# Kernel tuning notes

Hardware: AMD Instinct MI355X
Metric: run time of the kernel (lower is better)

The kernel has to match this reference:

```python
import jax, jax.numpy as jnp
import numpy as np

NB, B, IN, HID = 8, 256, 512, 512
G = 4 * HID
WB, IB, ABNM = 8, 8, 8
NL = 0.05


def quant(x, bits, r):
    # QuantFunc.forward: scale, clamp to (-1+1/step, 1-1/step), round to step grid, rescale
    step = 2.0 ** (bits - 1)
    x01 = jnp.clip(x / r, -1.0 + 1.0 / step, 1.0 - 1.0 / step)
    return jnp.round(x01 * step) / step * r


def pact(x, a):
    # pact_a_bmm vectorized over the block dim: sign(x)*0.5*(|x| - ||x|-a| + a)
    a3 = a[:, None, None]
    return jnp.sign(x) * 0.5 * (jnp.abs(x) - jnp.abs(jnp.abs(x) - a3) + a3)


def custom_mm(inp, w, b, nw, nb):
    # CustomMM_bmm.forward: quantize weights/bias (range 1.0), add scaled noise, bmm
    wq = quant(w, WB, 1.0)
    bq = quant(b, WB, 1.0)
    out = jnp.einsum('bni,bio->bno', inp, wq + nw * jnp.max(w) * NL)
    return out + bq + nb * jnp.max(b) * NL


def setup_inputs():
    key = jax.random.key(0)
    ks = jax.random.split(key, 11)
    inp = {
        'input': jax.random.normal(ks[0], (B, IN), jnp.float32),
        'hx': jax.random.normal(ks[1], (NB, B, HID), jnp.float32),
        'cx': jax.random.normal(ks[2], (NB, B, HID), jnp.float32),
        'weight_ih': jax.random.normal(ks[3], (NB, IN, G), jnp.float32),
        'weight_hh': jax.random.normal(ks[4], (NB, HID, G), jnp.float32),
        'bias_ih': jax.random.normal(ks[5], (NB, 1, G), jnp.float32),
        'bias_hh': jax.random.normal(ks[6], (NB, 1, G), jnp.float32),
        'noise_wih': jax.random.normal(ks[7], (NB, IN, G), jnp.float32),
        'noise_whh': jax.random.normal(ks[8], (NB, HID, G), jnp.float32),
        'noise_bih': jax.random.normal(ks[9], (NB, 1, G), jnp.float32),
        'noise_bhh': jax.random.normal(ks[10], (NB, 1, G), jnp.float32),
        'a1': jnp.full((NB,), 128.0, jnp.float32),
        'a3': jnp.ones((NB,), jnp.float32),
        'a4': jnp.ones((NB,), jnp.float32),
        'a5': jnp.ones((NB,), jnp.float32),
        'a6': jnp.ones((NB,), jnp.float32),
        'a7': jnp.full((NB,), 4.0, jnp.float32),
        'a8': jnp.ones((NB,), jnp.float32),
        'a9': jnp.full((NB,), 4.0, jnp.float32),
        'a10': jnp.ones((NB,), jnp.float32),
        'a11': jnp.full((NB,), 4.0, jnp.float32),
    }
    return inp


def reference(input, hx, cx, weight_ih, weight_hh, bias_ih, bias_hh,
              noise_wih, noise_whh, noise_bih, noise_bhh,
              a1, a3, a4, a5, a6, a7, a8, a9, a10, a11):
    xr = jnp.broadcast_to(input[None], (NB,) + input.shape)  # input.repeat(n_blocks,1,1)
    xq = quant(pact(xr, a1), IB, a1[:, None, None])
    gates = custom_mm(xq, weight_ih, bias_ih, noise_wih, noise_bih) \
          + custom_mm(hx, weight_hh, bias_hh, noise_whh, noise_bhh)
    i, j, f, o = jnp.split(gates, 4, axis=2)
    qp = lambda x, a: quant(pact(x, a), ABNM, a[:, None, None])
    fg = qp(jax.nn.sigmoid(f), a3)
    ig = qp(jax.nn.sigmoid(i), a4)
    act = qp(jnp.tanh(j), a5)
    og = qp(jax.nn.sigmoid(o), a6)
    gated = qp(cx * fg, a7)
    actin = qp(ig * act, a8)
    new_c = qp(gated + actin, a9)
    actc = qp(jnp.tanh(new_c), a10)
    new_h = qp(actc * og, a11)
    return new_h, new_c
```

## Files before the change

### kernel.cpp

```cpp
#include <hip/hip_runtime.h>
#include <hip/hip_bf16.h>

#define NBATCH 8
#define BROWS 256
#define KDIM 512
#define HIDD 512
#define GDIM 2048

typedef float f32x4 __attribute__((ext_vector_type(4)));
typedef __bf16 bf16x8 __attribute__((ext_vector_type(8)));

__device__ __forceinline__ unsigned fenc(float f) {
    unsigned u = __float_as_uint(f);
    return (u & 0x80000000u) ? ~u : (u | 0x80000000u);
}
__device__ __forceinline__ float fdec(unsigned e) {
    unsigned u = (e & 0x80000000u) ? (e & 0x7fffffffu) : ~e;
    return __uint_as_float(u);
}
__device__ __forceinline__ unsigned umaxu(unsigned a, unsigned b) { return a > b ? a : b; }

__device__ __forceinline__ float qpact(float x, float a) {
    float ax = fabsf(x);
    float p  = copysignf(0.5f * (ax - fabsf(ax - a) + a), x);
    float x01 = p / a;
    x01 = fminf(fmaxf(x01, -0.9921875f), 0.9921875f);
    return (rintf(x01 * 128.f) * 0.0078125f) * a;
}
__device__ __forceinline__ float q1(float x) {
    float x01 = fminf(fmaxf(x, -0.9921875f), 0.9921875f);
    return rintf(x01 * 128.f) * 0.0078125f;
}
__device__ __forceinline__ float sigmf(float x) { return 1.0f / (1.0f + expf(-x)); }

__global__ void k_init(unsigned* m) { if (threadIdx.x < 4) m[threadIdx.x] = 0u; }

__global__ void k_max(const float* __restrict__ w_ih, const float* __restrict__ w_hh,
                      const float* __restrict__ b_ih, const float* __restrict__ b_hh,
                      unsigned* __restrict__ omax) {
    int which = blockIdx.y;
    const float* src = which == 0 ? w_ih : which == 1 ? w_hh : which == 2 ? b_ih : b_hh;
    int n4 = (which < 2 ? NBATCH * KDIM * GDIM : NBATCH * GDIM) >> 2;
    unsigned best = 0u;
    int stride = gridDim.x * blockDim.x;
    for (int i = blockIdx.x * blockDim.x + threadIdx.x; i < n4; i += stride) {
        float4 v = ((const float4*)src)[i];
        best = umaxu(best, fenc(v.x)); best = umaxu(best, fenc(v.y));
        best = umaxu(best, fenc(v.z)); best = umaxu(best, fenc(v.w));
    }
    #pragma unroll
    for (int off = 32; off > 0; off >>= 1)
        best = umaxu(best, (unsigned)__shfl_down((int)best, off, 64));
    __shared__ unsigned red[4];
    int lane = threadIdx.x & 63, wv = threadIdx.x >> 6;
    if (lane == 0) red[wv] = best;
    __syncthreads();
    if (threadIdx.x == 0) {
        unsigned b2 = umaxu(umaxu(red[0], red[1]), umaxu(red[2], red[3]));
        atomicMax(&omax[which], b2);
    }
}

__global__ void k_prep(const float* __restrict__ input, const float* __restrict__ hx,
                       const float* __restrict__ bih, const float* __restrict__ bhh,
                       const float* __restrict__ nbih, const float* __restrict__ nbhh,
                       const float* __restrict__ a1, const unsigned* __restrict__ maxes,
                       __hip_bfloat16* __restrict__ xqh, __hip_bfloat16* __restrict__ hxh,
                       __hip_bfloat16* __restrict__ hxl, float* __restrict__ bias_comb) {
    const int NX = NBATCH * BROWS * KDIM;
    const int NH = NBATCH * BROWS * HIDD;
    const int NBC = NBATCH * GDIM;
    int total = NX + NH + NBC;
    int stride = gridDim.x * blockDim.x;
    for (int i = blockIdx.x * blockDim.x + threadIdx.x; i < total; i += stride) {
        if (i < NX) {
            int nb = i >> 17;
            int rem = i & 131071;
            float v = qpact(input[rem], a1[nb]);
            xqh[i] = __float2bfloat16(v);
        } else if (i < NX + NH) {
            int j = i - NX;
            float h = hx[j];
            __hip_bfloat16 hi = __float2bfloat16(h);
            hxh[j] = hi;
            hxl[j] = __float2bfloat16(h - __bfloat162float(hi));
        } else {
            int j = i - NX - NH;
            float mb_ih = fdec(maxes[2]);
            float mb_hh = fdec(maxes[3]);
            bias_comb[j] = q1(bih[j]) + (nbih[j] * mb_ih) * 0.05f
                         + q1(bhh[j]) + (nbhh[j] * mb_hh) * 0.05f;
        }
    }
}

__global__ __launch_bounds__(512) void k_gemm(
    const float* __restrict__ w_ih, const float* __restrict__ w_hh,
    const float* __restrict__ n_ih, const float* __restrict__ n_hh,
    const __hip_bfloat16* __restrict__ xqh, const __hip_bfloat16* __restrict__ hxh,
    const __hip_bfloat16* __restrict__ hxl,
    const float* __restrict__ bias_comb, const float* __restrict__ cx,
    const float* __restrict__ a3, const float* __restrict__ a4, const float* __restrict__ a5,
    const float* __restrict__ a6, const float* __restrict__ a7, const float* __restrict__ a8,
    const float* __restrict__ a9, const float* __restrict__ a10, const float* __restrict__ a11,
    const unsigned* __restrict__ maxes,
    float* __restrict__ out_h, float* __restrict__ out_c)
{
    __shared__ __hip_bfloat16 Bsm[4][64][40];

    int tid = threadIdx.x;
    int lane = tid & 63, wv = tid >> 6;
    int nb = blockIdx.x >> 5;
    int cb = blockIdx.x & 31;

    const float* wih_b = w_ih + nb * KDIM * GDIM;
    const float* whh_b = w_hh + nb * KDIM * GDIM;
    const float* nih_b = n_ih + nb * KDIM * GDIM;
    const float* nhh_b = n_hh + nb * KDIM * GDIM;
    const __hip_bfloat16* xq_b = xqh + nb * BROWS * KDIM;
    const __hip_bfloat16* hh_b = hxh + nb * BROWS * KDIM;
    const __hip_bfloat16* hl_b = hxl + nb * BROWS * KDIM;

    float c_ih = fdec(maxes[0]);
    float c_hh = fdec(maxes[1]);

    f32x4 acc[2][4] = {};

    int lh = lane & 15;
    int lk = (lane >> 4) << 3;
    int m0 = wv << 5;

    for (int k0 = 0; k0 < KDIM; k0 += 32) {
        __syncthreads();
        #pragma unroll
        for (int t = 0; t < 4; ++t) {
            int id = tid + (t << 9);
            int n = id & 63;
            int k = id >> 6;
            int g = n >> 4;
            int col = (g << 9) + (cb << 4) + (n & 15);
            int gidx = (k0 + k) * GDIM + col;
            float w1 = wih_b[gidx], z1 = nih_b[gidx];
            float wq1 = rintf(fminf(fmaxf(w1, -0.9921875f), 0.9921875f) * 128.f) * 0.0078125f;
            float e1 = wq1 + (z1 * c_ih) * 0.05f;
            __hip_bfloat16 h1 = __float2bfloat16(e1);
            Bsm[0][n][k] = h1;
            Bsm[1][n][k] = __float2bfloat16(e1 - __bfloat162float(h1));
            float w2 = whh_b[gidx], z2 = nhh_b[gidx];
            float wq2 = rintf(fminf(fmaxf(w2, -0.9921875f), 0.9921875f) * 128.f) * 0.0078125f;
            float e2 = wq2 + (z2 * c_hh) * 0.05f;
            __hip_bfloat16 h2 = __float2bfloat16(e2);
            Bsm[2][n][k] = h2;
            Bsm[3][n][k] = __float2bfloat16(e2 - __bfloat162float(h2));
        }
        __syncthreads();

        bf16x8 ax[2], ah[2], al[2];
        #pragma unroll
        for (int mf = 0; mf < 2; ++mf) {
            int r = m0 + (mf << 4) + lh;
            int aoff = r * KDIM + k0 + lk;
            ax[mf] = *(const bf16x8*)(xq_b + aoff);
            ah[mf] = *(const bf16x8*)(hh_b + aoff);
            al[mf] = *(const bf16x8*)(hl_b + aoff);
        }
        bf16x8 b0[4], b1[4], b2[4], b3[4];
        #pragma unroll
        for (int nf = 0; nf < 4; ++nf) {
            int n = (nf << 4) + lh;
            b0[nf] = *(const bf16x8*)&Bsm[0][n][lk];
            b1[nf] = *(const bf16x8*)&Bsm[1][n][lk];
            b2[nf] = *(const bf16x8*)&Bsm[2][n][lk];
            b3[nf] = *(const bf16x8*)&Bsm[3][n][lk];
        }
        #pragma unroll
        for (int mf = 0; mf < 2; ++mf)
            #pragma unroll
            for (int nf = 0; nf < 4; ++nf) {
                acc[mf][nf] = __builtin_amdgcn_mfma_f32_16x16x32_bf16(ax[mf], b0[nf], acc[mf][nf], 0, 0, 0);
                acc[mf][nf] = __builtin_amdgcn_mfma_f32_16x16x32_bf16(ax[mf], b1[nf], acc[mf][nf], 0, 0, 0);
                acc[mf][nf] = __builtin_amdgcn_mfma_f32_16x16x32_bf16(ah[mf], b2[nf], acc[mf][nf], 0, 0, 0);
                acc[mf][nf] = __builtin_amdgcn_mfma_f32_16x16x32_bf16(ah[mf], b3[nf], acc[mf][nf], 0, 0, 0);
                acc[mf][nf] = __builtin_amdgcn_mfma_f32_16x16x32_bf16(al[mf], b2[nf], acc[mf][nf], 0, 0, 0);
            }
    }

    int hcol = (cb << 4) + lh;
    float A3 = a3[nb], A4 = a4[nb], A5 = a5[nb], A6 = a6[nb], A7 = a7[nb];
    float A8 = a8[nb], A9 = a9[nb], A10 = a10[nb], A11 = a11[nb];
    float bc_i = bias_comb[nb * GDIM + hcol];
    float bc_j = bias_comb[nb * GDIM + 512 + hcol];
    float bc_f = bias_comb[nb * GDIM + 1024 + hcol];
    float bc_o = bias_comb[nb * GDIM + 1536 + hcol];
    #pragma unroll
    for (int mf = 0; mf < 2; ++mf)
        #pragma unroll
        for (int rg = 0; rg < 4; ++rg) {
            int r = m0 + (mf << 4) + ((lane >> 4) << 2) + rg;
            float gi = acc[mf][0][rg] + bc_i;
            float gj = acc[mf][1][rg] + bc_j;
            float gf = acc[mf][2][rg] + bc_f;
            float go = acc[mf][3][rg] + bc_o;
            float fg = qpact(sigmf(gf), A3);
            float ig = qpact(sigmf(gi), A4);
            float act = qpact(tanhf(gj), A5);
            float og = qpact(sigmf(go), A6);
            int oidx = (nb * BROWS + r) * HIDD + hcol;
            float cv = cx[oidx];
            float gated = qpact(cv * fg, A7);
            float actin = qpact(ig * act, A8);
            float ncv = qpact(gated + actin, A9);
            float acv = qpact(tanhf(ncv), A10);
            float nhv = qpact(acv * og, A11);
            out_h[oidx] = nhv;
            out_c[oidx] = ncv;
        }
}

extern "C" void kernel_launch(void* const* d_in, const int* in_sizes, int n_in,
                              void* d_out, int out_size, void* d_ws, size_t ws_size,
                              hipStream_t stream) {
    const float* input = (const float*)d_in[0];
    const float* hx    = (const float*)d_in[1];
    const float* cx    = (const float*)d_in[2];
    const float* w_ih  = (const float*)d_in[3];
    const float* w_hh  = (const float*)d_in[4];
    const float* b_ih  = (const float*)d_in[5];
    const float* b_hh  = (const float*)d_in[6];
    const float* n_wih = (const float*)d_in[7];
    const float* n_whh = (const float*)d_in[8];
    const float* n_bih = (const float*)d_in[9];
    const float* n_bhh = (const float*)d_in[10];
    const float* a1  = (const float*)d_in[11];
    const float* a3  = (const float*)d_in[12];
    const float* a4  = (const float*)d_in[13];
    const float* a5  = (const float*)d_in[14];
    const float* a6  = (const float*)d_in[15];
    const float* a7  = (const float*)d_in[16];
    const float* a8  = (const float*)d_in[17];
    const float* a9  = (const float*)d_in[18];
    const float* a10 = (const float*)d_in[19];
    const float* a11 = (const float*)d_in[20];

    float* out_h = (float*)d_out;
    float* out_c = out_h + NBATCH * BROWS * HIDD;

    char* ws = (char*)d_ws;
    unsigned* maxes = (unsigned*)ws;
    __hip_bfloat16* xqh = (__hip_bfloat16*)(ws + 256);
    __hip_bfloat16* hxh = (__hip_bfloat16*)(ws + 256 + 2097152);
    __hip_bfloat16* hxl = (__hip_bfloat16*)(ws + 256 + 2 * 2097152);
    float* bias_comb    = (float*)(ws + 256 + 3 * 2097152);

    k_init<<<1, 64, 0, stream>>>(maxes);
    k_max<<<dim3(256, 4), 256, 0, stream>>>(w_ih, w_hh, b_ih, b_hh, maxes);
    k_prep<<<2048, 256, 0, stream>>>(input, hx, b_ih, b_hh, n_bih, n_bhh, a1, maxes,
                                     xqh, hxh, hxl, bias_comb);
    k_gemm<<<NBATCH * 32, 512, 0, stream>>>(w_ih, w_hh, n_wih, n_whh, xqh, hxh, hxl,
                                            bias_comb, cx,
                                            a3, a4, a5, a6, a7, a8, a9, a10, a11,
                                            maxes, out_h, out_c);
}
```

Before: 97.91 us.

## Double-buffer weight staging with register prefetch and vectorized float4 loads in k_gemm

Reworks the GEMM main loop so weight and noise tiles are loaded as float4 vectors into registers two k-steps ahead. They are then quantized into one of two shared-memory buffers, so only one barrier is needed per k-step instead of two. The block index mapping is also swapped so that consecutive blocks cover different NB batches, and launch bounds now request two blocks per CU. The aim is to hide global-load latency behind the MFMA work, at the cost of doubled LDS use and higher register pressure.

```diff
diff --git a/kernel.cpp b/kernel.cpp
--- a/kernel.cpp
+++ b/kernel.cpp
@@ -6,6 +6,8 @@
 #define KDIM 512
 #define HIDD 512
 #define GDIM 2048
+#define KSTEP 32
+#define NIT (KDIM / KSTEP)
 
 typedef float f32x4 __attribute__((ext_vector_type(4)));
 typedef __bf16 bf16x8 __attribute__((ext_vector_type(8)));
@@ -94,7 +96,7 @@
     }
 }
 
-__global__ __launch_bounds__(512) void k_gemm(
+__global__ __launch_bounds__(512, 2) void k_gemm(
     const float* __restrict__ w_ih, const float* __restrict__ w_hh,
     const float* __restrict__ n_ih, const float* __restrict__ n_hh,
     const __hip_bfloat16* __restrict__ xqh, const __hip_bfloat16* __restrict__ hxh,
@@ -106,12 +108,12 @@
     const unsigned* __restrict__ maxes,
     float* __restrict__ out_h, float* __restrict__ out_c)
 {
-    __shared__ __hip_bfloat16 Bsm[4][64][40];
+    __shared__ __hip_bfloat16 Bsm[2][4][64][40];
 
     int tid = threadIdx.x;
     int lane = tid & 63, wv = tid >> 6;
-    int nb = blockIdx.x >> 5;
-    int cb = blockIdx.x & 31;
+    int nb = blockIdx.x & 7;
+    int cb = blockIdx.x >> 3;
 
     const float* wih_b = w_ih + nb * KDIM * GDIM;
     const float* whh_b = w_hh + nb * KDIM * GDIM;
@@ -130,59 +132,79 @@
     int lk = (lane >> 4) << 3;
     int m0 = wv << 5;
 
-    for (int k0 = 0; k0 < KDIM; k0 += 32) {
+    int sn0 = (tid & 15) << 2;
+    int sk  = tid >> 4;
+    int scol = ((sn0 >> 4) << 9) + (cb << 4) + (sn0 & 15);
+    int sbase = sk * GDIM + scol;
+
+    f32x4 rw1a, rz1a, rw2a, rz2a;
+    f32x4 rw1b, rz1b, rw2b, rz2b;
+    bf16x8 axv[2], ahv[2], alv[2];
+
+#define STAGE(RW1, RZ1, RW2, RZ2, K0) {            \
+    int gx = sbase + (K0) * GDIM;                  \
+    RW1 = *(const f32x4*)(wih_b + gx);             \
+    RZ1 = *(const f32x4*)(nih_b + gx);             \
+    RW2 = *(const f32x4*)(whh_b + gx);             \
+    RZ2 = *(const f32x4*)(nhh_b + gx); }
+
+#define ALOAD(K0) {                                \
+    _Pragma("unroll")                              \
+    for (int mf = 0; mf < 2; ++mf) {               \
+        int aoff = (m0 + (mf << 4) + lh) * KDIM + (K0) + lk; \
+        axv[mf] = *(const bf16x8*)(xq_b + aoff);   \
+        ahv[mf] = *(const bf16x8*)(hh_b + aoff);   \
+        alv[mf] = *(const bf16x8*)(hl_b + aoff); } }
+
+#define CVT(P, RW1, RZ1, RW2, RZ2) {               \
+    _Pragma("unroll")                              \
+    for (int j = 0; j < 4; ++j) {                  \
+        float w1 = RW1[j], z1 = RZ1[j];            \
+        float wq1 = rintf(fminf(fmaxf(w1, -0.9921875f), 0.9921875f) * 128.f) * 0.0078125f; \
+        float e1 = wq1 + (z1 * c_ih) * 0.05f;      \
+        __hip_bfloat16 h1 = __float2bfloat16(e1);  \
+        Bsm[P][0][sn0 + j][sk] = h1;               \
+        Bsm[P][1][sn0 + j][sk] = __float2bfloat16(e1 - __bfloat162float(h1)); \
+        float w2 = RW2[j], z2 = RZ2[j];            \
+        float wq2 = rintf(fminf(fmaxf(w2, -0.9921875f), 0.9921875f) * 128.f) * 0.0078125f; \
+        float e2 = wq2 + (z2 * c_hh) * 0.05f;      \
+        __hip_bfloat16 h2 = __float2bfloat16(e2);  \
+        Bsm[P][2][sn0 + j][sk] = h2;               \
+        Bsm[P][3][sn0 + j][sk] = __float2bfloat16(e2 - __bfloat162float(h2)); \
+    } }
+
+#define COMPUTE(P) {                               \
+    _Pragma("unroll")                              \
+    for (int nf = 0; nf < 4; ++nf) {               \
+        int n = (nf << 4) + lh;                    \
+        bf16x8 b0 = *(const bf16x8*)&Bsm[P][0][n][lk]; \
+        bf16x8 b1 = *(const bf16x8*)&Bsm[P][1][n][lk]; \
+        bf16x8 b2 = *(const bf16x8*)&Bsm[P][2][n][lk]; \
+        bf16x8 b3 = *(const bf16x8*)&Bsm[P][3][n][lk]; \
+        _Pragma("unroll")                          \
+        for (int mf = 0; mf < 2; ++mf) {           \
+            acc[mf][nf] = __builtin_amdgcn_mfma_f32_16x16x32_bf16(axv[mf], b0, acc[mf][nf], 0, 0, 0); \
+            acc[mf][nf] = __builtin_amdgcn_mfma_f32_16x16x32_bf16(axv[mf], b1, acc[mf][nf], 0, 0, 0); \
+            acc[mf][nf] = __builtin_amdgcn_mfma_f32_16x16x32_bf16(ahv[mf], b2, acc[mf][nf], 0, 0, 0); \
+            acc[mf][nf] = __builtin_amdgcn_mfma_f32_16x16x32_bf16(ahv[mf], b3, acc[mf][nf], 0, 0, 0); \
+            acc[mf][nf] = __builtin_amdgcn_mfma_f32_16x16x32_bf16(alv[mf], b2, acc[mf][nf], 0, 0, 0); \
+        } \
+    } }
+
+    STAGE(rw1a, rz1a, rw2a, rz2a, 0);
+    STAGE(rw1b, rz1b, rw2b, rz2b, KSTEP);
+
+    for (int it = 0; it < NIT; it += 2) {
+        ALOAD(it * KSTEP);
+        CVT(0, rw1a, rz1a, rw2a, rz2a);
+        if (it + 2 < NIT) STAGE(rw1a, rz1a, rw2a, rz2a, (it + 2) * KSTEP);
         __syncthreads();
-        #pragma unroll
-        for (int t = 0; t < 4; ++t) {
-            int id = tid + (t << 9);
-            int n = id & 63;
-            int k = id >> 6;
-            int g = n >> 4;
-            int col = (g << 9) + (cb << 4) + (n & 15);
-            int gidx = (k0 + k) * GDIM + col;
-            float w1 = wih_b[gidx], z1 = nih_b[gidx];
-            float wq1 = rintf(fminf(fmaxf(w1, -0.9921875f), 0.9921875f) * 128.f) * 0.0078125f;
-            float e1 = wq1 + (z1 * c_ih) * 0.05f;
-            __hip_bfloat16 h1 = __float2bfloat16(e1);
-            Bsm[0][n][k] = h1;
-            Bsm[1][n][k] = __float2bfloat16(e1 - __bfloat162float(h1));
-            float w2 = whh_b[gidx], z2 = nhh_b[gidx];
-            float wq2 = rintf(fminf(fmaxf(w2, -0.9921875f), 0.9921875f) * 128.f) * 0.0078125f;
-            float e2 = wq2 + (z2 * c_hh) * 0.05f;
-            __hip_bfloat16 h2 = __float2bfloat16(e2);
-            Bsm[2][n][k] = h2;
-            Bsm[3][n][k] = __float2bfloat16(e2 - __bfloat162float(h2));
-        }
+        COMPUTE(0);
+        ALOAD((it + 1) * KSTEP);
+        CVT(1, rw1b, rz1b, rw2b, rz2b);
+        if (it + 3 < NIT) STAGE(rw1b, rz1b, rw2b, rz2b, (it + 3) * KSTEP);
         __syncthreads();
-
-        bf16x8 ax[2], ah[2], al[2];
-        #pragma unroll
-        for (int mf = 0; mf < 2; ++mf) {
-            int r = m0 + (mf << 4) + lh;
-            int aoff = r * KDIM + k0 + lk;
-            ax[mf] = *(const bf16x8*)(xq_b + aoff);
-            ah[mf] = *(const bf16x8*)(hh_b + aoff);
-            al[mf] = *(const bf16x8*)(hl_b + aoff);
-        }
-        bf16x8 b0[4], b1[4], b2[4], b3[4];
-        #pragma unroll
-        for (int nf = 0; nf < 4; ++nf) {
-            int n = (nf << 4) + lh;
-            b0[nf] = *(const bf16x8*)&Bsm[0][n][lk];
-            b1[nf] = *(const bf16x8*)&Bsm[1][n][lk];
-            b2[nf] = *(const bf16x8*)&Bsm[2][n][lk];
-            b3[nf] = *(const bf16x8*)&Bsm[3][n][lk];
-        }
-        #pragma unroll
-        for (int mf = 0; mf < 2; ++mf)
-            #pragma unroll
-            for (int nf = 0; nf < 4; ++nf) {
-                acc[mf][nf] = __builtin_amdgcn_mfma_f32_16x16x32_bf16(ax[mf], b0[nf], acc[mf][nf], 0, 0, 0);
-                acc[mf][nf] = __builtin_amdgcn_mfma_f32_16x16x32_bf16(ax[mf], b1[nf], acc[mf][nf], 0, 0, 0);
-                acc[mf][nf] = __builtin_amdgcn_mfma_f32_16x16x32_bf16(ah[mf], b2[nf], acc[mf][nf], 0, 0, 0);
-                acc[mf][nf] = __builtin_amdgcn_mfma_f32_16x16x32_bf16(ah[mf], b3[nf], acc[mf][nf], 0, 0, 0);
-                acc[mf][nf] = __builtin_amdgcn_mfma_f32_16x16x32_bf16(al[mf], b2[nf], acc[mf][nf], 0, 0, 0);
-            }
+        COMPUTE(1);
     }
 
     int hcol = (cb << 4) + lh;
```

New measurement: 80.19 us. 18.1% less time.

## Warp-specialize GEMM with producer waves double-buffering weight conversion into LDS

Applied to the files above, without the earlier changes.

Splits each 1024-thread block into 8 producer waves, which load, quantize and split weights into a double-buffered LDS tile, and 8 consumer waves, which run 32x32x16 MFMAs on the previous tile. Global weight loads and conversion now overlap with matrix math, and KSTEP goes to 64. The block-to-tile mapping is swizzled so adjacent blocks cover different batches, and the init kernel becomes a memset. The epilogue uses cross-lane shuffles to regroup gate columns. The risk is that a single 1024-thread block per CU limits occupancy and adds register pressure.

```diff
diff --git a/kernel.cpp b/kernel.cpp
--- a/kernel.cpp
+++ b/kernel.cpp
@@ -6,8 +6,11 @@
 #define KDIM 512
 #define HIDD 512
 #define GDIM 2048
+#define KSTEP 64
+#define NIT (KDIM / KSTEP)
 
 typedef float f32x4 __attribute__((ext_vector_type(4)));
+typedef float f32x16 __attribute__((ext_vector_type(16)));
 typedef __bf16 bf16x8 __attribute__((ext_vector_type(8)));
 
 __device__ __forceinline__ unsigned fenc(float f) {
@@ -32,8 +35,6 @@
     return rintf(x01 * 128.f) * 0.0078125f;
 }
 __device__ __forceinline__ float sigmf(float x) { return 1.0f / (1.0f + expf(-x)); }
-
-__global__ void k_init(unsigned* m) { if (threadIdx.x < 4) m[threadIdx.x] = 0u; }
 
 __global__ void k_max(const float* __restrict__ w_ih, const float* __restrict__ w_hh,
                       const float* __restrict__ b_ih, const float* __restrict__ b_hh,
@@ -94,7 +95,7 @@
     }
 }
 
-__global__ __launch_bounds__(512) void k_gemm(
+__global__ __launch_bounds__(1024, 1) void k_gemm(
     const float* __restrict__ w_ih, const float* __restrict__ w_hh,
     const float* __restrict__ n_ih, const float* __restrict__ n_hh,
     const __hip_bfloat16* __restrict__ xqh, const __hip_bfloat16* __restrict__ hxh,
@@ -106,12 +107,12 @@
     const unsigned* __restrict__ maxes,
     float* __restrict__ out_h, float* __restrict__ out_c)
 {
-    __shared__ __hip_bfloat16 Bsm[4][64][40];
+    __shared__ __hip_bfloat16 Bsm[2][4][64][72];
 
     int tid = threadIdx.x;
     int lane = tid & 63, wv = tid >> 6;
-    int nb = blockIdx.x >> 5;
-    int cb = blockIdx.x & 31;
+    int nb = blockIdx.x & 7;
+    int cb = blockIdx.x >> 3;
 
     const float* wih_b = w_ih + nb * KDIM * GDIM;
     const float* whh_b = w_hh + nb * KDIM * GDIM;
@@ -124,88 +125,128 @@
     float c_ih = fdec(maxes[0]);
     float c_hh = fdec(maxes[1]);
 
-    f32x4 acc[2][4] = {};
-
-    int lh = lane & 15;
-    int lk = (lane >> 4) << 3;
-    int m0 = wv << 5;
-
-    for (int k0 = 0; k0 < KDIM; k0 += 32) {
-        __syncthreads();
-        #pragma unroll
-        for (int t = 0; t < 4; ++t) {
-            int id = tid + (t << 9);
-            int n = id & 63;
-            int k = id >> 6;
-            int g = n >> 4;
-            int col = (g << 9) + (cb << 4) + (n & 15);
-            int gidx = (k0 + k) * GDIM + col;
-            float w1 = wih_b[gidx], z1 = nih_b[gidx];
-            float wq1 = rintf(fminf(fmaxf(w1, -0.9921875f), 0.9921875f) * 128.f) * 0.0078125f;
-            float e1 = wq1 + (z1 * c_ih) * 0.05f;
-            __hip_bfloat16 h1 = __float2bfloat16(e1);
-            Bsm[0][n][k] = h1;
-            Bsm[1][n][k] = __float2bfloat16(e1 - __bfloat162float(h1));
-            float w2 = whh_b[gidx], z2 = nhh_b[gidx];
-            float wq2 = rintf(fminf(fmaxf(w2, -0.9921875f), 0.9921875f) * 128.f) * 0.0078125f;
-            float e2 = wq2 + (z2 * c_hh) * 0.05f;
-            __hip_bfloat16 h2 = __float2bfloat16(e2);
-            Bsm[2][n][k] = h2;
-            Bsm[3][n][k] = __float2bfloat16(e2 - __bfloat162float(h2));
+    bool producer = wv >= 8;
+
+    int pn = lane;
+    int po = (wv - 8) & 7;
+    int ps = pn >> 4;
+    int gm = (int)((0x3120u >> (ps << 2)) & 0xFu);
+    int pcol = (gm << 9) + (cb << 4) + (pn & 15);
+
+    int cw = wv & 7;
+    int c31 = lane & 31;
+    int ck8 = (lane >> 5) << 3;
+
+    f32x16 acc0 = {}, acc1 = {};
+    float rw1[8], rz1[8], rw2[8], rz2[8];
+
+#define PSTAGE(K0) {                                         \
+    int kb = (K0) + (po << 3);                               \
+    _Pragma("unroll")                                        \
+    for (int j = 0; j < 8; ++j) {                            \
+        int gx = (kb + j) * GDIM + pcol;                     \
+        rw1[j] = wih_b[gx]; rz1[j] = nih_b[gx];              \
+        rw2[j] = whh_b[gx]; rz2[j] = nhh_b[gx];              \
+    } }
+
+#define PCVT1(P, RW, RZ, CM, MHI) {                          \
+    bf16x8 hi8, lo8;                                         \
+    _Pragma("unroll")                                        \
+    for (int j = 0; j < 8; ++j) {                            \
+        float w = RW[j];                                     \
+        float wq = rintf(fminf(fmaxf(w, -0.9921875f), 0.9921875f) * 128.f) * 0.0078125f; \
+        float e = wq + (RZ[j] * (CM)) * 0.05f;               \
+        __hip_bfloat16 h = __float2bfloat16(e);              \
+        float lof = e - __bfloat162float(h);                 \
+        __hip_bfloat16 lb = __float2bfloat16(lof);           \
+        hi8[j] = *reinterpret_cast<__bf16*>(&h);             \
+        lo8[j] = *reinterpret_cast<__bf16*>(&lb);            \
+    }                                                        \
+    *(bf16x8*)&Bsm[P][MHI][pn][po << 3] = hi8;               \
+    *(bf16x8*)&Bsm[P][(MHI) + 1][pn][po << 3] = lo8; }
+
+#define MFMA5(ACC, AX, AH, AL, B0, B1, B2, B3)                                \
+    ACC = __builtin_amdgcn_mfma_f32_32x32x16_bf16(AX, B0, ACC, 0, 0, 0);      \
+    ACC = __builtin_amdgcn_mfma_f32_32x32x16_bf16(AX, B1, ACC, 0, 0, 0);      \
+    ACC = __builtin_amdgcn_mfma_f32_32x32x16_bf16(AH, B2, ACC, 0, 0, 0);      \
+    ACC = __builtin_amdgcn_mfma_f32_32x32x16_bf16(AH, B3, ACC, 0, 0, 0);      \
+    ACC = __builtin_amdgcn_mfma_f32_32x32x16_bf16(AL, B2, ACC, 0, 0, 0);
+
+    if (producer) PSTAGE(0);
+
+    for (int ph = 0; ph <= NIT; ++ph) {
+        if (producer) {
+            if (ph < NIT) {
+                int P = ph & 1;
+                PCVT1(P, rw1, rz1, c_ih, 0);
+                PCVT1(P, rw2, rz2, c_hh, 2);
+                if (ph + 1 < NIT) PSTAGE((ph + 1) * KSTEP);
+            }
+        } else if (ph > 0) {
+            int K0 = (ph - 1) * KSTEP;
+            int P = (ph - 1) & 1;
+            bf16x8 ax[4], ah[4], al[4];
+            int abase = (cw * 32 + c31) * KDIM + K0 + ck8;
+            #pragma unroll
+            for (int kc = 0; kc < 4; ++kc) {
+                ax[kc] = *(const bf16x8*)(xq_b + abase + kc * 16);
+                ah[kc] = *(const bf16x8*)(hh_b + abase + kc * 16);
+                al[kc] = *(const bf16x8*)(hl_b + abase + kc * 16);
+            }
+            #pragma unroll
+            for (int kc = 0; kc < 4; ++kc) {
+                int kb = kc * 16 + ck8;
+                {
+                    bf16x8 b0 = *(const bf16x8*)&Bsm[P][0][c31][kb];
+                    bf16x8 b1 = *(const bf16x8*)&Bsm[P][1][c31][kb];
+                    bf16x8 b2 = *(const bf16x8*)&Bsm[P][2][c31][kb];
+                    bf16x8 b3 = *(const bf16x8*)&Bsm[P][3][c31][kb];
+                    MFMA5(acc0, ax[kc], ah[kc], al[kc], b0, b1, b2, b3);
+                }
+                {
+                    bf16x8 b0 = *(const bf16x8*)&Bsm[P][0][32 + c31][kb];
+                    bf16x8 b1 = *(const bf16x8*)&Bsm[P][1][32 + c31][kb];
+                    bf16x8 b2 = *(const bf16x8*)&Bsm[P][2][32 + c31][kb];
+                    bf16x8 b3 = *(const bf16x8*)&Bsm[P][3][32 + c31][kb];
+                    MFMA5(acc1, ax[kc], ah[kc], al[kc], b0, b1, b2, b3);
+                }
+            }
         }
         __syncthreads();
-
-        bf16x8 ax[2], ah[2], al[2];
+    }
+
+    if (!producer) {
+        float recv0[16], recv1[16];
         #pragma unroll
-        for (int mf = 0; mf < 2; ++mf) {
-            int r = m0 + (mf << 4) + lh;
-            int aoff = r * KDIM + k0 + lk;
-            ax[mf] = *(const bf16x8*)(xq_b + aoff);
-            ah[mf] = *(const bf16x8*)(hh_b + aoff);
-            al[mf] = *(const bf16x8*)(hl_b + aoff);
+        for (int r = 0; r < 16; ++r) {
+            recv0[r] = __shfl_xor(acc0[r], 16);
+            recv1[r] = __shfl_xor(acc1[r], 16);
         }
-        bf16x8 b0[4], b1[4], b2[4], b3[4];
+        int hcol = (cb << 4) + (lane & 15);
+        int hi = (lane >> 4) & 1;
+        float A3 = a3[nb], A4 = a4[nb], A5 = a5[nb], A6 = a6[nb], A7 = a7[nb];
+        float A8 = a8[nb], A9 = a9[nb], A10 = a10[nb], A11 = a11[nb];
+        float bc_i = bias_comb[nb * GDIM + hcol];
+        float bc_j = bias_comb[nb * GDIM + 512 + hcol];
+        float bc_f = bias_comb[nb * GDIM + 1024 + hcol];
+        float bc_o = bias_comb[nb * GDIM + 1536 + hcol];
+        int rbase = 16 * hi + 4 * (lane >> 5);
         #pragma unroll
-        for (int nf = 0; nf < 4; ++nf) {
-            int n = (nf << 4) + lh;
-            b0[nf] = *(const bf16x8*)&Bsm[0][n][lk];
-            b1[nf] = *(const bf16x8*)&Bsm[1][n][lk];
-            b2[nf] = *(const bf16x8*)&Bsm[2][n][lk];
-            b3[nf] = *(const bf16x8*)&Bsm[3][n][lk];
-        }
-        #pragma unroll
-        for (int mf = 0; mf < 2; ++mf)
-            #pragma unroll
-            for (int nf = 0; nf < 4; ++nf) {
-                acc[mf][nf] = __builtin_amdgcn_mfma_f32_16x16x32_bf16(ax[mf], b0[nf], acc[mf][nf], 0, 0, 0);
-                acc[mf][nf] = __builtin_amdgcn_mfma_f32_16x16x32_bf16(ax[mf], b1[nf], acc[mf][nf], 0, 0, 0);
-                acc[mf][nf] = __builtin_amdgcn_mfma_f32_16x16x32_bf16(ah[mf], b2[nf], acc[mf][nf], 0, 0, 0);
-                acc[mf][nf] = __builtin_amdgcn_mfma_f32_16x16x32_bf16(ah[mf], b3[nf], acc[mf][nf], 0, 0, 0);
-                acc[mf][nf] = __builtin_amdgcn_mfma_f32_16x16x32_bf16(al[mf], b2[nf], acc[mf][nf], 0, 0, 0);
-            }
-    }
-
-    int hcol = (cb << 4) + lh;
-    float A3 = a3[nb], A4 = a4[nb], A5 = a5[nb], A6 = a6[nb], A7 = a7[nb];
-    float A8 = a8[nb], A9 = a9[nb], A10 = a10[nb], A11 = a11[nb];
-    float bc_i = bias_comb[nb * GDIM + hcol];
-    float bc_j = bias_comb[nb * GDIM + 512 + hcol];
-    float bc_f = bias_comb[nb * GDIM + 1024 + hcol];
-    float bc_o = bias_comb[nb * GDIM + 1536 + hcol];
-    #pragma unroll
-    for (int mf = 0; mf < 2; ++mf)
-        #pragma unroll
-        for (int rg = 0; rg < 4; ++rg) {
-            int r = m0 + (mf << 4) + ((lane >> 4) << 2) + rg;
-            float gi = acc[mf][0][rg] + bc_i;
-            float gj = acc[mf][1][rg] + bc_j;
-            float gf = acc[mf][2][rg] + bc_f;
-            float go = acc[mf][3][rg] + bc_o;
+        for (int r = 0; r < 8; ++r) {
+            float a0s = hi ? acc0[r + 8] : acc0[r];
+            float a1s = hi ? acc1[r + 8] : acc1[r];
+            float r0s = hi ? recv0[r + 8] : recv0[r];
+            float r1s = hi ? recv1[r + 8] : recv1[r];
+            float gi = (hi ? r0s : a0s) + bc_i;
+            float gj = (hi ? r1s : a1s) + bc_j;
+            float gf = (hi ? a0s : r0s) + bc_f;
+            float go = (hi ? a1s : r1s) + bc_o;
+            int row = cw * 32 + rbase + (r & 3) + 8 * (r >> 2);
             float fg = qpact(sigmf(gf), A3);
             float ig = qpact(sigmf(gi), A4);
             float act = qpact(tanhf(gj), A5);
             float og = qpact(sigmf(go), A6);
-            int oidx = (nb * BROWS + r) * HIDD + hcol;
+            int oidx = (nb * BROWS + row) * HIDD + hcol;
             float cv = cx[oidx];
             float gated = qpact(cv * fg, A7);
             float actin = qpact(ig * act, A8);
@@ -215,6 +256,7 @@
             out_h[oidx] = nhv;
             out_c[oidx] = ncv;
         }
+    }
 }
 
 extern "C" void kernel_launch(void* const* d_in, const int* in_sizes, int n_in,
@@ -252,12 +294,12 @@
     __hip_bfloat16* hxl = (__hip_bfloat16*)(ws + 256 + 2 * 2097152);
     float* bias_comb    = (float*)(ws + 256 + 3 * 2097152);
 
-    k_init<<<1, 64, 0, stream>>>(maxes);
+    hipMemsetAsync(maxes, 0, 16, stream);
     k_max<<<dim3(256, 4), 256, 0, stream>>>(w_ih, w_hh, b_ih, b_hh, maxes);
     k_prep<<<2048, 256, 0, stream>>>(input, hx, b_ih, b_hh, n_bih, n_bhh, a1, maxes,
                                      xqh, hxh, hxl, bias_comb);
-    k_gemm<<<NBATCH * 32, 512, 0, stream>>>(w_ih, w_hh, n_wih, n_whh, xqh, hxh, hxl,
-                                            bias_comb, cx,
-                                            a3, a4, a5, a6, a7, a8, a9, a10, a11,
-                                            maxes, out_h, out_c);
-}
+    k_gemm<<<NBATCH * 32, 1024, 0, stream>>>(w_ih, w_hh, n_wih, n_whh, xqh, hxh, hxl,
+                                             bias_comb, cx,
+                                             a3, a4, a5, a6, a7, a8, a9, a10, a11,
+                                             maxes, out_h, out_c);
+}
```

Result: faster. 93.07 us (-4.9%).

## Prepack quantized weights into tiled bf16 buffer and double-buffer GEMM via LDS loads

Applied to the files above, without the earlier changes.

Moves the weight quantize, noise add and hi/lo bf16 split out of the GEMM into a separate pack kernel that writes a tiled, padded layout to workspace. The GEMM then streams those tiles with global_load_lds into double-buffered shared memory, uses 32x32x16 MFMAs, and stages results through LDS for a coalesced epilogue. The max-reduction and activation prep kernels are merged and the init kernel becomes a memset. This adds an extra write and read of a packed weight buffer (about 32 MB of bf16) in exchange for a GEMM main loop with no fp32 weight reads or conversion.

```diff
diff --git a/kernel.cpp b/kernel.cpp
--- a/kernel.cpp
+++ b/kernel.cpp
@@ -7,8 +7,26 @@
 #define HIDD 512
 #define GDIM 2048
 
+#define ROWB 144
+#define MATSZ (64 * ROWB)
+#define PCHUNK (4 * MATSZ)
+#define NPH 8
+
+#define WS_XQH 256
+#define WS_HXH (256 + 2097152)
+#define WS_HXL (256 + 2 * 2097152)
+#define WS_BIAS (256 + 3 * 2097152)
+#define WS_P (256 + 3 * 2097152 + 65536)
+
 typedef float f32x4 __attribute__((ext_vector_type(4)));
+typedef float f32x16 __attribute__((ext_vector_type(16)));
 typedef __bf16 bf16x8 __attribute__((ext_vector_type(8)));
+typedef unsigned int u32;
+
+__device__ __forceinline__ void gload16(const void* g, void* l) {
+    __builtin_amdgcn_global_load_lds((const __attribute__((address_space(1))) u32*)g,
+                                     (__attribute__((address_space(3))) u32*)l, 16, 0, 0);
+}
 
 __device__ __forceinline__ unsigned fenc(float f) {
     unsigned u = __float_as_uint(f);
@@ -33,159 +51,216 @@
 }
 __device__ __forceinline__ float sigmf(float x) { return 1.0f / (1.0f + expf(-x)); }
 
-__global__ void k_init(unsigned* m) { if (threadIdx.x < 4) m[threadIdx.x] = 0u; }
-
-__global__ void k_max(const float* __restrict__ w_ih, const float* __restrict__ w_hh,
-                      const float* __restrict__ b_ih, const float* __restrict__ b_hh,
-                      unsigned* __restrict__ omax) {
-    int which = blockIdx.y;
-    const float* src = which == 0 ? w_ih : which == 1 ? w_hh : which == 2 ? b_ih : b_hh;
-    int n4 = (which < 2 ? NBATCH * KDIM * GDIM : NBATCH * GDIM) >> 2;
-    unsigned best = 0u;
+__global__ void k_maxprep(const float* __restrict__ w_ih, const float* __restrict__ w_hh,
+                          const float* __restrict__ b_ih, const float* __restrict__ b_hh,
+                          const float* __restrict__ input, const float* __restrict__ hx,
+                          const float* __restrict__ a1,
+                          unsigned* __restrict__ maxes,
+                          __hip_bfloat16* __restrict__ xqh, __hip_bfloat16* __restrict__ hxh,
+                          __hip_bfloat16* __restrict__ hxl) {
+    int y = blockIdx.y;
     int stride = gridDim.x * blockDim.x;
-    for (int i = blockIdx.x * blockDim.x + threadIdx.x; i < n4; i += stride) {
-        float4 v = ((const float4*)src)[i];
-        best = umaxu(best, fenc(v.x)); best = umaxu(best, fenc(v.y));
-        best = umaxu(best, fenc(v.z)); best = umaxu(best, fenc(v.w));
-    }
-    #pragma unroll
-    for (int off = 32; off > 0; off >>= 1)
-        best = umaxu(best, (unsigned)__shfl_down((int)best, off, 64));
-    __shared__ unsigned red[4];
-    int lane = threadIdx.x & 63, wv = threadIdx.x >> 6;
-    if (lane == 0) red[wv] = best;
-    __syncthreads();
-    if (threadIdx.x == 0) {
-        unsigned b2 = umaxu(umaxu(red[0], red[1]), umaxu(red[2], red[3]));
-        atomicMax(&omax[which], b2);
-    }
-}
-
-__global__ void k_prep(const float* __restrict__ input, const float* __restrict__ hx,
-                       const float* __restrict__ bih, const float* __restrict__ bhh,
-                       const float* __restrict__ nbih, const float* __restrict__ nbhh,
-                       const float* __restrict__ a1, const unsigned* __restrict__ maxes,
-                       __hip_bfloat16* __restrict__ xqh, __hip_bfloat16* __restrict__ hxh,
-                       __hip_bfloat16* __restrict__ hxl, float* __restrict__ bias_comb) {
-    const int NX = NBATCH * BROWS * KDIM;
-    const int NH = NBATCH * BROWS * HIDD;
-    const int NBC = NBATCH * GDIM;
-    int total = NX + NH + NBC;
-    int stride = gridDim.x * blockDim.x;
-    for (int i = blockIdx.x * blockDim.x + threadIdx.x; i < total; i += stride) {
-        if (i < NX) {
-            int nb = i >> 17;
-            int rem = i & 131071;
-            float v = qpact(input[rem], a1[nb]);
-            xqh[i] = __float2bfloat16(v);
-        } else if (i < NX + NH) {
-            int j = i - NX;
-            float h = hx[j];
-            __hip_bfloat16 hi = __float2bfloat16(h);
-            hxh[j] = hi;
-            hxl[j] = __float2bfloat16(h - __bfloat162float(hi));
-        } else {
-            int j = i - NX - NH;
-            float mb_ih = fdec(maxes[2]);
-            float mb_hh = fdec(maxes[3]);
-            bias_comb[j] = q1(bih[j]) + (nbih[j] * mb_ih) * 0.05f
-                         + q1(bhh[j]) + (nbhh[j] * mb_hh) * 0.05f;
-        }
-    }
-}
-
-__global__ __launch_bounds__(512) void k_gemm(
+    int gtid = blockIdx.x * blockDim.x + threadIdx.x;
+    if (y < 4) {
+        const float* src = y == 0 ? w_ih : y == 1 ? w_hh : y == 2 ? b_ih : b_hh;
+        int n4 = (y < 2 ? NBATCH * KDIM * GDIM : NBATCH * GDIM) >> 2;
+        unsigned best = 0u;
+        for (int i = gtid; i < n4; i += stride) {
+            float4 v = ((const float4*)src)[i];
+            best = umaxu(best, fenc(v.x)); best = umaxu(best, fenc(v.y));
+            best = umaxu(best, fenc(v.z)); best = umaxu(best, fenc(v.w));
+        }
+        #pragma unroll
+        for (int off = 32; off > 0; off >>= 1)
+            best = umaxu(best, (unsigned)__shfl_down((int)best, off, 64));
+        __shared__ unsigned red[4];
+        int lane = threadIdx.x & 63, wv = threadIdx.x >> 6;
+        if (lane == 0) red[wv] = best;
+        __syncthreads();
+        if (threadIdx.x == 0) {
+            unsigned b2 = umaxu(umaxu(red[0], red[1]), umaxu(red[2], red[3]));
+            atomicMax(&maxes[y], b2);
+        }
+    } else {
+        const int NX = NBATCH * BROWS * KDIM;
+        const int NH = NBATCH * BROWS * HIDD;
+        int total = NX + NH;
+        for (int i = gtid; i < total; i += stride) {
+            if (i < NX) {
+                int nb = i >> 17;
+                int rem = i & 131071;
+                float v = qpact(input[rem], a1[nb]);
+                xqh[i] = __float2bfloat16(v);
+            } else {
+                int j = i - NX;
+                float h = hx[j];
+                __hip_bfloat16 hi = __float2bfloat16(h);
+                hxh[j] = hi;
+                hxl[j] = __float2bfloat16(h - __bfloat162float(hi));
+            }
+        }
+    }
+}
+
+__global__ __launch_bounds__(1024) void k_pack(
     const float* __restrict__ w_ih, const float* __restrict__ w_hh,
     const float* __restrict__ n_ih, const float* __restrict__ n_hh,
+    const float* __restrict__ b_ih, const float* __restrict__ b_hh,
+    const float* __restrict__ nbih, const float* __restrict__ nbhh,
+    const unsigned* __restrict__ maxes,
+    char* __restrict__ P, float* __restrict__ bias_comb) {
+    int bid = blockIdx.x;
+    if (bid == 256) {
+        float mb_ih = fdec(maxes[2]);
+        float mb_hh = fdec(maxes[3]);
+        #pragma unroll
+        for (int it = 0; it < 16; ++it) {
+            int j = it * 1024 + threadIdx.x;
+            bias_comb[j] = q1(b_ih[j]) + (nbih[j] * mb_ih) * 0.05f
+                         + q1(b_hh[j]) + (nbhh[j] * mb_hh) * 0.05f;
+        }
+        return;
+    }
+    int nb = bid >> 5;
+    int p  = (bid >> 1) & 15;
+    int ch = bid & 1;
+    int k0 = p * 32;
+    int ph = p >> 1;
+    int half = p & 1;
+    float c_ih = fdec(maxes[0]);
+    float c_hh = fdec(maxes[1]);
+
+    int c = ch * 1024 + threadIdx.x;
+    int g  = c >> 9;
+    int cw = c & 511;
+    int cb = cw >> 4;
+    int cc = cw & 15;
+    int n  = (g << 4) + cc;
+
+    char* rowP = P + ((size_t)((nb * 32 + cb) * 8 + ph)) * PCHUNK + n * ROWB + half * 64;
+    size_t boff = (size_t)nb * KDIM * GDIM;
+
+    #pragma unroll
+    for (int pair = 0; pair < 2; ++pair) {
+        const float* W = (pair ? w_hh : w_ih) + boff;
+        const float* Z = (pair ? n_hh : n_ih) + boff;
+        float cm = pair ? c_hh : c_ih;
+        char* dhi = rowP + (pair * 2) * MATSZ;
+        char* dlo = rowP + (pair * 2 + 1) * MATSZ;
+        #pragma unroll
+        for (int c4 = 0; c4 < 4; ++c4) {
+            bf16x8 hi8, lo8;
+            #pragma unroll
+            for (int j = 0; j < 8; ++j) {
+                int k = k0 + c4 * 8 + j;
+                float w = W[(size_t)k * GDIM + c];
+                float z = Z[(size_t)k * GDIM + c];
+                float wq = rintf(fminf(fmaxf(w, -0.9921875f), 0.9921875f) * 128.f) * 0.0078125f;
+                float e = wq + (z * cm) * 0.05f;
+                __hip_bfloat16 h = __float2bfloat16(e);
+                float lof = e - __bfloat162float(h);
+                __hip_bfloat16 lb = __float2bfloat16(lof);
+                hi8[j] = *reinterpret_cast<__bf16*>(&h);
+                lo8[j] = *reinterpret_cast<__bf16*>(&lb);
+            }
+            *(bf16x8*)(dhi + c4 * 16) = hi8;
+            *(bf16x8*)(dlo + c4 * 16) = lo8;
+        }
+    }
+}
+
+__global__ __launch_bounds__(512, 2) void k_gemm(
+    const char* __restrict__ P,
     const __hip_bfloat16* __restrict__ xqh, const __hip_bfloat16* __restrict__ hxh,
     const __hip_bfloat16* __restrict__ hxl,
     const float* __restrict__ bias_comb, const float* __restrict__ cx,
     const float* __restrict__ a3, const float* __restrict__ a4, const float* __restrict__ a5,
     const float* __restrict__ a6, const float* __restrict__ a7, const float* __restrict__ a8,
     const float* __restrict__ a9, const float* __restrict__ a10, const float* __restrict__ a11,
-    const unsigned* __restrict__ maxes,
     float* __restrict__ out_h, float* __restrict__ out_c)
 {
-    __shared__ __hip_bfloat16 Bsm[4][64][40];
+    __shared__ __align__(16) char Tl[2][PCHUNK];
+    __shared__ float Gx[4][256][16];
 
     int tid = threadIdx.x;
-    int lane = tid & 63, wv = tid >> 6;
-    int nb = blockIdx.x >> 5;
-    int cb = blockIdx.x & 31;
-
-    const float* wih_b = w_ih + nb * KDIM * GDIM;
-    const float* whh_b = w_hh + nb * KDIM * GDIM;
-    const float* nih_b = n_ih + nb * KDIM * GDIM;
-    const float* nhh_b = n_hh + nb * KDIM * GDIM;
+    int lane = tid & 63, w = tid >> 6;
+    int l31 = lane & 31, l5 = lane >> 5;
+    int nb = blockIdx.x & 7;
+    int cb = blockIdx.x >> 3;
+    int mband = w & 3;
+    int cg = w >> 2;
+
+    const char* Pblk = P + (size_t)(nb * 32 + cb) * 8 * PCHUNK;
     const __hip_bfloat16* xq_b = xqh + nb * BROWS * KDIM;
     const __hip_bfloat16* hh_b = hxh + nb * BROWS * KDIM;
     const __hip_bfloat16* hl_b = hxl + nb * BROWS * KDIM;
 
-    float c_ih = fdec(maxes[0]);
-    float c_hh = fdec(maxes[1]);
-
-    f32x4 acc[2][4] = {};
-
-    int lh = lane & 15;
-    int lk = (lane >> 4) << 3;
-    int m0 = wv << 5;
-
-    for (int k0 = 0; k0 < KDIM; k0 += 32) {
+    f32x16 acc0 = {}, acc1 = {};
+    int row0 = mband * 64 + l31;
+
+#define STAGE(BUF, PH) {                                                     \
+    const char* src = Pblk + (size_t)(PH) * PCHUNK;                          \
+    _Pragma("unroll")                                                        \
+    for (int t = 0; t < 5; ++t) {                                            \
+        if (t * 8 + w < 36) {                                                \
+            int off = t * 8192 + w * 1024;                                   \
+            gload16(src + off + lane * 16, &Tl[BUF][off]);                   \
+        }                                                                    \
+    } }
+
+#define MFMA(ACC, A, B) ACC = __builtin_amdgcn_mfma_f32_32x32x16_bf16(A, B, ACC, 0, 0, 0)
+
+    STAGE(0, 0);
+    __syncthreads();
+    int cur = 0;
+
+    for (int ph = 0; ph < NPH; ++ph) {
+        bf16x8 ax[2][4], ah[2][4], al[2][4];
+        #pragma unroll
+        for (int kc = 0; kc < 4; ++kc) {
+            int k = ph * 64 + kc * 16 + l5 * 8;
+            #pragma unroll
+            for (int mi = 0; mi < 2; ++mi) {
+                int r = row0 + mi * 32;
+                ax[mi][kc] = *(const bf16x8*)(xq_b + r * KDIM + k);
+                ah[mi][kc] = *(const bf16x8*)(hh_b + r * KDIM + k);
+                al[mi][kc] = *(const bf16x8*)(hl_b + r * KDIM + k);
+            }
+        }
+        if (ph + 1 < NPH) STAGE(cur ^ 1, ph + 1);
+
+        const char* Tb = Tl[cur];
+        int nrow = cg * 32 + l31;
+        #pragma unroll
+        for (int kc = 0; kc < 4; ++kc) {
+            int bo = nrow * ROWB + kc * 32 + l5 * 16;
+            bf16x8 b0 = *(const bf16x8*)(Tb + 0 * MATSZ + bo);
+            bf16x8 b1 = *(const bf16x8*)(Tb + 1 * MATSZ + bo);
+            bf16x8 b2 = *(const bf16x8*)(Tb + 2 * MATSZ + bo);
+            bf16x8 b3 = *(const bf16x8*)(Tb + 3 * MATSZ + bo);
+            MFMA(acc0, ax[0][kc], b0); MFMA(acc0, ax[0][kc], b1);
+            MFMA(acc0, ah[0][kc], b2); MFMA(acc0, ah[0][kc], b3);
+            MFMA(acc0, al[0][kc], b2);
+            MFMA(acc1, ax[1][kc], b0); MFMA(acc1, ax[1][kc], b1);
+            MFMA(acc1, ah[1][kc], b2); MFMA(acc1, ah[1][kc], b3);
+            MFMA(acc1, al[1][kc], b2);
+        }
         __syncthreads();
-        #pragma unroll
-        for (int t = 0; t < 4; ++t) {
-            int id = tid + (t << 9);
-            int n = id & 63;
-            int k = id >> 6;
-            int g = n >> 4;
-            int col = (g << 9) + (cb << 4) + (n & 15);
-            int gidx = (k0 + k) * GDIM + col;
-            float w1 = wih_b[gidx], z1 = nih_b[gidx];
-            float wq1 = rintf(fminf(fmaxf(w1, -0.9921875f), 0.9921875f) * 128.f) * 0.0078125f;
-            float e1 = wq1 + (z1 * c_ih) * 0.05f;
-            __hip_bfloat16 h1 = __float2bfloat16(e1);
-            Bsm[0][n][k] = h1;
-            Bsm[1][n][k] = __float2bfloat16(e1 - __bfloat162float(h1));
-            float w2 = whh_b[gidx], z2 = nhh_b[gidx];
-            float wq2 = rintf(fminf(fmaxf(w2, -0.9921875f), 0.9921875f) * 128.f) * 0.0078125f;
-            float e2 = wq2 + (z2 * c_hh) * 0.05f;
-            __hip_bfloat16 h2 = __float2bfloat16(e2);
-            Bsm[2][n][k] = h2;
-            Bsm[3][n][k] = __float2bfloat16(e2 - __bfloat162float(h2));
-        }
-        __syncthreads();
-
-        bf16x8 ax[2], ah[2], al[2];
-        #pragma unroll
-        for (int mf = 0; mf < 2; ++mf) {
-            int r = m0 + (mf << 4) + lh;
-            int aoff = r * KDIM + k0 + lk;
-            ax[mf] = *(const bf16x8*)(xq_b + aoff);
-            ah[mf] = *(const bf16x8*)(hh_b + aoff);
-            al[mf] = *(const bf16x8*)(hl_b + aoff);
-        }
-        bf16x8 b0[4], b1[4], b2[4], b3[4];
-        #pragma unroll
-        for (int nf = 0; nf < 4; ++nf) {
-            int n = (nf << 4) + lh;
-            b0[nf] = *(const bf16x8*)&Bsm[0][n][lk];
-            b1[nf] = *(const bf16x8*)&Bsm[1][n][lk];
-            b2[nf] = *(const bf16x8*)&Bsm[2][n][lk];
-            b3[nf] = *(const bf16x8*)&Bsm[3][n][lk];
-        }
-        #pragma unroll
-        for (int mf = 0; mf < 2; ++mf)
-            #pragma unroll
-            for (int nf = 0; nf < 4; ++nf) {
-                acc[mf][nf] = __builtin_amdgcn_mfma_f32_16x16x32_bf16(ax[mf], b0[nf], acc[mf][nf], 0, 0, 0);
-                acc[mf][nf] = __builtin_amdgcn_mfma_f32_16x16x32_bf16(ax[mf], b1[nf], acc[mf][nf], 0, 0, 0);
-                acc[mf][nf] = __builtin_amdgcn_mfma_f32_16x16x32_bf16(ah[mf], b2[nf], acc[mf][nf], 0, 0, 0);
-                acc[mf][nf] = __builtin_amdgcn_mfma_f32_16x16x32_bf16(ah[mf], b3[nf], acc[mf][nf], 0, 0, 0);
-                acc[mf][nf] = __builtin_amdgcn_mfma_f32_16x16x32_bf16(al[mf], b2[nf], acc[mf][nf], 0, 0, 0);
-            }
-    }
-
-    int hcol = (cb << 4) + lh;
+        cur ^= 1;
+    }
+
+    int gq = (cg * 32 + l31) >> 4;
+    int hq = l31 & 15;
+    #pragma unroll
+    for (int r = 0; r < 16; ++r) {
+        int rw = mband * 64 + (r & 3) + 8 * (r >> 2) + 4 * l5;
+        Gx[gq][rw][hq] = acc0[r];
+        Gx[gq][rw + 32][hq] = acc1[r];
+    }
+    __syncthreads();
+
+    int h = tid & 15;
+    int hcol = cb * 16 + h;
     float A3 = a3[nb], A4 = a4[nb], A5 = a5[nb], A6 = a6[nb], A7 = a7[nb];
     float A8 = a8[nb], A9 = a9[nb], A10 = a10[nb], A11 = a11[nb];
     float bc_i = bias_comb[nb * GDIM + hcol];
@@ -193,28 +268,26 @@
     float bc_f = bias_comb[nb * GDIM + 1024 + hcol];
     float bc_o = bias_comb[nb * GDIM + 1536 + hcol];
     #pragma unroll
-    for (int mf = 0; mf < 2; ++mf)
-        #pragma unroll
-        for (int rg = 0; rg < 4; ++rg) {
-            int r = m0 + (mf << 4) + ((lane >> 4) << 2) + rg;
-            float gi = acc[mf][0][rg] + bc_i;
-            float gj = acc[mf][1][rg] + bc_j;
-            float gf = acc[mf][2][rg] + bc_f;
-            float go = acc[mf][3][rg] + bc_o;
-            float fg = qpact(sigmf(gf), A3);
-            float ig = qpact(sigmf(gi), A4);
-            float act = qpact(tanhf(gj), A5);
-            float og = qpact(sigmf(go), A6);
-            int oidx = (nb * BROWS + r) * HIDD + hcol;
-            float cv = cx[oidx];
-            float gated = qpact(cv * fg, A7);
-            float actin = qpact(ig * act, A8);
-            float ncv = qpact(gated + actin, A9);
-            float acv = qpact(tanhf(ncv), A10);
-            float nhv = qpact(acv * og, A11);
-            out_h[oidx] = nhv;
-            out_c[oidx] = ncv;
-        }
+    for (int s = 0; s < 8; ++s) {
+        int row = s * 32 + (tid >> 4);
+        float gi = Gx[0][row][h] + bc_i;
+        float gj = Gx[1][row][h] + bc_j;
+        float gf = Gx[2][row][h] + bc_f;
+        float go = Gx[3][row][h] + bc_o;
+        float fg = qpact(sigmf(gf), A3);
+        float ig = qpact(sigmf(gi), A4);
+        float act = qpact(tanhf(gj), A5);
+        float og = qpact(sigmf(go), A6);
+        int oidx = (nb * BROWS + row) * HIDD + hcol;
+        float cv = cx[oidx];
+        float gated = qpact(cv * fg, A7);
+        float actin = qpact(ig * act, A8);
+        float ncv = qpact(gated + actin, A9);
+        float acv = qpact(tanhf(ncv), A10);
+        float nhv = qpact(acv * og, A11);
+        out_h[oidx] = nhv;
+        out_c[oidx] = ncv;
+    }
 }
 
 extern "C" void kernel_launch(void* const* d_in, const int* in_sizes, int n_in,
@@ -247,17 +320,18 @@
 
     char* ws = (char*)d_ws;
     unsigned* maxes = (unsigned*)ws;
-    __hip_bfloat16* xqh = (__hip_bfloat16*)(ws + 256);
-    __hip_bfloat16* hxh = (__hip_bfloat16*)(ws + 256 + 2097152);
-    __hip_bfloat16* hxl = (__hip_bfloat16*)(ws + 256 + 2 * 2097152);
-    float* bias_comb    = (float*)(ws + 256 + 3 * 2097152);
-
-    k_init<<<1, 64, 0, stream>>>(maxes);
-    k_max<<<dim3(256, 4), 256, 0, stream>>>(w_ih, w_hh, b_ih, b_hh, maxes);
-    k_prep<<<2048, 256, 0, stream>>>(input, hx, b_ih, b_hh, n_bih, n_bhh, a1, maxes,
-                                     xqh, hxh, hxl, bias_comb);
-    k_gemm<<<NBATCH * 32, 512, 0, stream>>>(w_ih, w_hh, n_wih, n_whh, xqh, hxh, hxl,
-                                            bias_comb, cx,
+    __hip_bfloat16* xqh = (__hip_bfloat16*)(ws + WS_XQH);
+    __hip_bfloat16* hxh = (__hip_bfloat16*)(ws + WS_HXH);
+    __hip_bfloat16* hxl = (__hip_bfloat16*)(ws + WS_HXL);
+    float* bias_comb    = (float*)(ws + WS_BIAS);
+    char* P             = ws + WS_P;
+
+    hipMemsetAsync(maxes, 0, 16, stream);
+    k_maxprep<<<dim3(256, 5), 256, 0, stream>>>(w_ih, w_hh, b_ih, b_hh, input, hx, a1,
+                                                maxes, xqh, hxh, hxl);
+    k_pack<<<257, 1024, 0, stream>>>(w_ih, w_hh, n_wih, n_whh, b_ih, b_hh, n_bih, n_bhh,
+                                     maxes, P, bias_comb);
+    k_gemm<<<NBATCH * 32, 512, 0, stream>>>(P, xqh, hxh, hxl, bias_comb, cx,
                                             a3, a4, a5, a6, a7, a8, a9, a10, a11,
-                                            maxes, out_h, out_c);
-}
+                                            out_h, out_c);
+}
```

Result: slower. 148.0 us (+51.2%).
